# Kernel tuning notes

Hardware: AMD Instinct MI355X
Metric: run time of the kernel (lower is better)

Reference implementation:

```python
import jax, jax.numpy as jnp
import numpy as np

GROUPS = 8   # GroupNorm groups
TOP_K = 2    # top-k routing
TEMP = 1.0   # gate temperature
EPS_GN = 1e-5


def conv1d(x, w, b=None):
    # x: (B,C,T), w: (Cout,Cin,K) -> (B,Cout,T), 'same' padding
    pad = (w.shape[-1] - 1) // 2
    y = jax.lax.conv_general_dilated(x, w, (1,), [(pad, pad)],
                                     dimension_numbers=('NCH', 'OIH', 'NCH'))
    return y if b is None else y + b[None, :, None]


def group_norm(x, gamma, beta, groups=GROUPS, eps=EPS_GN):
    B, C, T = x.shape
    xg = x.reshape(B, groups, C // groups, T)
    mu = xg.mean((2, 3), keepdims=True)
    var = xg.var((2, 3), keepdims=True)
    xn = ((xg - mu) * jax.lax.rsqrt(var + eps)).reshape(B, C, T)
    return xn * gamma[None, :, None] + beta[None, :, None]


def layer_norm(x, gamma, beta, eps=EPS_GN):
    mu = x.mean(-1, keepdims=True)
    var = x.var(-1, keepdims=True)
    return (x - mu) * jax.lax.rsqrt(var + eps) * gamma + beta


def gelu(x):
    return jax.nn.gelu(x, approximate=False)  # torch nn.GELU default (erf)


def setup_inputs() -> dict:
    key = jax.random.key(0)
    ks = jax.random.split(key, 32)
    B, C, T = 32, 16, 2048
    E, CO, K = 8, 128, 5
    HID, CTX, DIN, DEMB = 128, 64, 8, 16
    GIN = CTX + DEMB
    n = lambda i, shape, s=0.05: jax.random.normal(ks[i], shape, dtype=jnp.float32) * s
    return {
        'x': jax.random.normal(ks[0], (B, C, T), dtype=jnp.float32),
        'demo': jax.random.normal(ks[1], (B, DIN), dtype=jnp.float32),
        # router context CNN (Conv1d no bias -> GroupNorm -> GELU)
        'rw': n(2, (HID, C, K)), 'rg': jnp.ones((HID,), jnp.float32), 'rb': jnp.zeros((HID,), jnp.float32),
        # router MLP: Linear -> LayerNorm -> GELU -> Linear
        'm1_w': n(3, (HID, HID)), 'm1_b': jnp.zeros((HID,), jnp.float32),
        'ln_g': jnp.ones((HID,), jnp.float32), 'ln_b': jnp.zeros((HID,), jnp.float32),
        'm2_w': n(4, (CTX, HID)), 'm2_b': jnp.zeros((CTX,), jnp.float32),
        # demographics embedder: Linear -> LayerNorm -> GELU -> Linear
        'd1_w': n(5, (2 * DEMB, DIN)), 'd1_b': jnp.zeros((2 * DEMB,), jnp.float32),
        'dln_g': jnp.ones((2 * DEMB,), jnp.float32), 'dln_b': jnp.zeros((2 * DEMB,), jnp.float32),
        'd2_w': n(6, (DEMB, 2 * DEMB)), 'd2_b': jnp.zeros((DEMB,), jnp.float32),
        # gate linear
        'g_w': n(7, (E, GIN)), 'g_b': jnp.zeros((E,), jnp.float32),
        # specialised expert CNNs (stacked over E): Conv1d -> GroupNorm -> GELU
        'ew': n(8, (E, CO, C, K)), 'eb': jnp.zeros((E, CO), jnp.float32),
        'eg': jnp.ones((E, CO), jnp.float32), 'ebt': jnp.zeros((E, CO), jnp.float32),
        # shared (always-on) expert CNN
        'sw': n(9, (CO, C, K)), 'sb': jnp.zeros((CO,), jnp.float32),
        'sg': jnp.ones((CO,), jnp.float32), 'sbt': jnp.zeros((CO,), jnp.float32),
    }


def reference(x, demo, rw, rg, rb, m1_w, m1_b, ln_g, ln_b, m2_w, m2_b,
              d1_w, d1_b, dln_g, dln_b, d2_w, d2_b, g_w, g_b,
              ew, eb, eg, ebt, sw, sb, sg, sbt):
    # ---- router: context CNN -> GAP -> MLP -> r (B, CTX)
    h = gelu(group_norm(conv1d(x, rw), rg, rb))
    r = h.mean(-1)  # GAP over time
    r = gelu(layer_norm(r @ m1_w.T + m1_b, ln_g, ln_b))
    r = r @ m2_w.T + m2_b
    # ---- demographics embedding, concat onto routing vector
    d = gelu(layer_norm(demo @ d1_w.T + d1_b, dln_g, dln_b))
    d = d @ d2_w.T + d2_b
    r = jnp.concatenate([r, d], axis=-1)  # (B, CTX+DEMB)
    # ---- gate: softmax + top-k mask + renormalise
    logits = (r @ g_w.T + g_b) / TEMP
    weights_soft = jax.nn.softmax(logits, axis=-1)  # (B, E)
    _, topk_idx = jax.lax.top_k(weights_soft, TOP_K)
    Bn = weights_soft.shape[0]
    mask = jnp.zeros_like(weights_soft).at[jnp.arange(Bn)[:, None], topk_idx].set(1.0)
    wh = weights_soft * mask
    weights_hard = wh / (wh.sum(-1, keepdims=True) + 1e-9)
    # ---- experts (dense compute, top-k-masked combine) + shared expert
    expert = lambda w, b, g, be: gelu(group_norm(conv1d(x, w, b), g, be))
    eo = jax.vmap(expert)(ew, eb, eg, ebt)  # (E, B, CO, T)
    shared = gelu(group_norm(conv1d(x, sw, sb), sg, sbt))  # (B, CO, T)
    out = shared + jnp.einsum('be,ebct->bct', weights_hard, eo)
    return out
```

## Files before the change

kernel.cpp:

```cpp
#include <hip/hip_runtime.h>
#include <math.h>

#define B_    32
#define CIN   16
#define T_    2048
#define NG    8
#define CPG   16
#define HID   128
#define KW    5
#define EPS_  1e-5f

#define NROW  2080
#define ROWS  16
#define NQ    4
#define QT    512
#define QROWS 544

#define SH_EWF  1064960
#define SH_RWF  1175552
#define FO_R0   593920
#define FO_GW   598016
#define FO_GI   598080
#define FO_STE  598144

typedef float f32x4 __attribute__((ext_vector_type(4)));
typedef short s16x8 __attribute__((ext_vector_type(8)));

__device__ __forceinline__ float gelu_fast(float y) {
    float p = y * y;
    float u = y * (0.7978845608028654f + 0.03567740813636141f * p);
    float au = fabsf(u);
    float e = __expf(2.0f * au);
    float th = copysignf(1.0f - 2.0f * __builtin_amdgcn_rcpf(e + 1.0f), u);
    return 0.5f * y * (1.0f + th);
}

__device__ __forceinline__ float gelu_sig(float y) {
    float e = __expf(-1.702f * y);
    return y * __builtin_amdgcn_rcpf(1.0f + e);
}

__device__ __forceinline__ float gelu_erf(float y) {
    return 0.5f * y * (1.0f + erff(y * 0.70710678118654752440f));
}

__device__ __forceinline__ short bf16r(float f) {
    unsigned u = __builtin_bit_cast(unsigned, f);
    u = u + 0x7FFFu + ((u >> 16) & 1u);
    return (short)(u >> 16);
}

__global__ __launch_bounds__(256) void prep_kernel(
    const float* __restrict__ x, const float* __restrict__ rw,
    const float* __restrict__ ew, const float* __restrict__ sw,
    short* __restrict__ wsf)
{
    const int bid = blockIdx.x, tid = threadIdx.x;
    if (bid < 64) {
        const int b = bid >> 1, half = bid & 1;
        const float* xb = x + (size_t)b * CIN * T_;
        short* xtb = wsf + (size_t)b * NROW * ROWS;
        const int t0 = (half * 256 + tid) * 4;

        float v[CIN][4];
        #pragma unroll
        for (int ci = 0; ci < CIN; ++ci)
            *(f32x4*)v[ci] = *(const f32x4*)(xb + ci * T_ + t0);

        #pragma unroll
        for (int tt = 0; tt < 4; ++tt) {
            s16x8 lo, hi;
            #pragma unroll
            for (int ci = 0; ci < 8; ++ci) lo[ci] = bf16r(v[ci][tt]);
            #pragma unroll
            for (int ci = 0; ci < 8; ++ci) hi[ci] = bf16r(v[ci + 8][tt]);
            short* rp = xtb + (size_t)(t0 + tt + 2) * ROWS;
            *(s16x8*)rp = lo;
            *(s16x8*)(rp + 8) = hi;
        }
        if (half == 0 && tid < 32) {
            int r = (tid < 2) ? tid : 2048 + tid;
            s16x8 z = {0, 0, 0, 0, 0, 0, 0, 0};
            short* rp = xtb + (size_t)r * ROWS;
            *(s16x8*)rp = z;
            *(s16x8*)(rp + 8) = z;
        }
    } else if (tid < 64) {
        const int id = bid - 64, l = tid;
        const int n = l & 15, grp = l >> 4;
        const int s_ = grp >> 1, cib = (grp & 1) * 8;
        const float* src;
        short* dst;
        if (id < 72) {
            int es = id / 8, g = id - es * 8;
            src = ((es == 0) ? sw : ew + (size_t)(es - 1) * 128 * (CIN * KW))
                  + (size_t)g * CPG * (CIN * KW);
            dst = wsf + SH_EWF + ((size_t)(es * 8 + g) * 3) * 64 * 8;
        } else {
            int g = id - 72;
            src = rw + (size_t)g * CPG * (CIN * KW);
            dst = wsf + SH_RWF + ((size_t)g * 3) * 64 * 8;
        }
        #pragma unroll
        for (int p = 0; p < 3; ++p) {
            int sh = 2 * p + s_;
            s16x8 a;
            if (sh < 5) {
                const float* wp = src + (size_t)n * (CIN * KW) + cib * KW + sh;
                #pragma unroll
                for (int j = 0; j < 8; ++j) a[j] = bf16r(wp[j * KW]);
            } else {
                #pragma unroll
                for (int j = 0; j < 8; ++j) a[j] = 0;
            }
            *(s16x8*)(dst + ((size_t)p * 64 + l) * 8) = a;
        }
    }
}

__device__ __forceinline__ void stage_xt_full(const short* __restrict__ xtb,
                                              short* __restrict__ xs, int tid)
{
    const s16x8* src = (const s16x8*)xtb;
    s16x8* dst = (s16x8*)xs;
    #pragma unroll
    for (int i = 0; i < 8; ++i)
        dst[tid + i * 512] = src[tid + i * 512];
    int i8 = tid + 8 * 512;
    if (i8 < NROW * 2) dst[i8] = src[i8];
}

__device__ __forceinline__ void stage_xt_q(const short* __restrict__ xtq,
                                           short* __restrict__ xs, int tid)
{
    const s16x8* src = (const s16x8*)xtq;
    s16x8* dst = (s16x8*)xs;
    #pragma unroll
    for (int i = 0; i < 4; ++i)
        dst[tid + i * 256] = src[tid + i * 256];
    int i4 = tid + 4 * 256;
    if (i4 < QROWS * 2) dst[i4] = src[i4];
}

__global__ __launch_bounds__(512, 4) void router_conv_kernel(
    const short* __restrict__ xt, const short* __restrict__ wsf,
    const float* __restrict__ rg, const float* __restrict__ rb,
    float* __restrict__ r0)
{
    __shared__ short xs[NROW * ROWS];
    __shared__ float redS[8], redQ[8];
    __shared__ float rsum[8][CPG];

    const int b = blockIdx.x, g = blockIdx.y;
    const int tid = threadIdx.x;
    const int l = tid & 63, wv = tid >> 6;
    const int n = l & 15, grp = l >> 4;
    const int s_ = grp >> 1;

    stage_xt_full(xt + (size_t)b * NROW * ROWS, xs, tid);

    const short* rwb = wsf + SH_RWF + ((size_t)g * 3) * 64 * 8;
    s16x8 afr0 = *(const s16x8*)(rwb + (0 * 64 + l) * 8);
    s16x8 afr1 = *(const s16x8*)(rwb + (1 * 64 + l) * 8);
    s16x8 afr2 = *(const s16x8*)(rwb + (2 * 64 + l) * 8);
    __syncthreads();

    const int cib = (grp & 1) * 8;
    f32x4 cst[16];
    float sA = 0.f, qA = 0.f;
    #pragma unroll
    for (int tile = 0; tile < 16; ++tile) {
        const int t0 = (wv * 16 + tile) * 16;
        s16x8 bf0 = *(const s16x8*)&xs[(t0 + n + 0 + s_) * ROWS + cib];
        s16x8 bf1 = *(const s16x8*)&xs[(t0 + n + 2 + s_) * ROWS + cib];
        s16x8 bf2 = *(const s16x8*)&xs[(t0 + n + 4 + s_) * ROWS + cib];
        f32x4 c = {0.f, 0.f, 0.f, 0.f};
        c = __builtin_amdgcn_mfma_f32_16x16x32_bf16(afr0, bf0, c, 0, 0, 0);
        c = __builtin_amdgcn_mfma_f32_16x16x32_bf16(afr1, bf1, c, 0, 0, 0);
        c = __builtin_amdgcn_mfma_f32_16x16x32_bf16(afr2, bf2, c, 0, 0, 0);
        cst[tile] = c;
        #pragma unroll
        for (int r = 0; r < 4; ++r) { sA += c[r]; qA += c[r] * c[r]; }
    }

    for (int d = 1; d < 64; d <<= 1) {
        sA += __shfl_xor(sA, d);
        qA += __shfl_xor(qA, d);
    }
    if (l == 0) { redS[wv] = sA; redQ[wv] = qA; }
    __syncthreads();
    float S = 0.f, Q = 0.f;
    for (int i = 0; i < 8; ++i) { S += redS[i]; Q += redQ[i]; }
    const float inv_n = 1.0f / (CPG * T_);
    float mu = S * inv_n;
    float rs = rsqrtf(Q * inv_n - mu * mu + EPS_);
    float ka[4], kb[4];
    #pragma unroll
    for (int r = 0; r < 4; ++r) {
        int co = g * CPG + grp * 4 + r;
        float gm = rg[co];
        ka[r] = rs * gm;
        kb[r] = rb[co] - mu * rs * gm;
    }

    f32x4 tacc = {0.f, 0.f, 0.f, 0.f};
    #pragma unroll
    for (int tile = 0; tile < 16; ++tile) {
        #pragma unroll
        for (int r = 0; r < 4; ++r)
            tacc[r] += gelu_fast(cst[tile][r] * ka[r] + kb[r]);
    }
    #pragma unroll
    for (int r = 0; r < 4; ++r)
        for (int d = 1; d < 16; d <<= 1)
            tacc[r] += __shfl_xor(tacc[r], d);
    if (n == 0) {
        #pragma unroll
        for (int r = 0; r < 4; ++r) rsum[wv][grp * 4 + r] = tacc[r];
    }
    __syncthreads();
    if (tid < CPG) {
        float a = 0.f;
        for (int w = 0; w < 8; ++w) a += rsum[w][tid];
        r0[b * HID + g * CPG + tid] = a * (1.0f / T_);
    }
}

__global__ void router_gate_kernel(
    const float* __restrict__ r0, const float* __restrict__ demo,
    const float* __restrict__ m1w, const float* __restrict__ m1b,
    const float* __restrict__ lng, const float* __restrict__ lnb,
    const float* __restrict__ m2w, const float* __restrict__ m2b,
    const float* __restrict__ d1w, const float* __restrict__ d1b,
    const float* __restrict__ dlng, const float* __restrict__ dlnb,
    const float* __restrict__ d2w, const float* __restrict__ d2b,
    const float* __restrict__ gw, const float* __restrict__ gb,
    float* __restrict__ gateW, int* __restrict__ gateI)
{
    __shared__ float sh[128];
    __shared__ float dd[32];
    __shared__ float rr[80];
    __shared__ float glds[8];
    __shared__ float red[2], redq[2];

    const int b = blockIdx.x;
    const int j = threadIdx.x;
    const int lane = j & 63, wv = j >> 6;

    sh[j] = r0[b * HID + j];
    __syncthreads();

    float v = m1b[j];
    for (int i = 0; i < 128; ++i) v += sh[i] * m1w[j * 128 + i];
    float s = v, sq = v * v;
    for (int d = 1; d < 64; d <<= 1) { s += __shfl_xor(s, d); sq += __shfl_xor(sq, d); }
    if (lane == 0) { red[wv] = s; redq[wv] = sq; }
    __syncthreads();
    float S = red[0] + red[1], SQ = redq[0] + redq[1];
    float mu = S * (1.f / 128.f), var = SQ * (1.f / 128.f) - mu * mu;
    float h = (v - mu) * rsqrtf(var + EPS_) * lng[j] + lnb[j];
    float gv = gelu_erf(h);
    __syncthreads();
    sh[j] = gv;
    __syncthreads();

    if (j < 64) {
        float rv = m2b[j];
        for (int i = 0; i < 128; ++i) rv += sh[i] * m2w[j * 128 + i];
        rr[j] = rv;
    } else if (j < 96) {
        int jd = j - 64;
        float u = d1b[jd];
        for (int i = 0; i < 8; ++i) u += demo[b * 8 + i] * d1w[jd * 8 + i];
        float s2 = u, q2 = u * u;
        for (int d = 1; d < 32; d <<= 1) { s2 += __shfl_xor(s2, d, 32); q2 += __shfl_xor(q2, d, 32); }
        float mu2 = s2 * (1.f / 32.f), var2 = q2 * (1.f / 32.f) - mu2 * mu2;
        float y = (u - mu2) * rsqrtf(var2 + EPS_) * dlng[jd] + dlnb[jd];
        dd[jd] = gelu_erf(y);
    }
    __syncthreads();
    if (j < 16) {
        float rv = d2b[j];
        for (int i = 0; i < 32; ++i) rv += dd[i] * d2w[j * 32 + i];
        rr[64 + j] = rv;
    }
    __syncthreads();
    if (j < 8) {
        float lg = gb[j];
        for (int i = 0; i < 80; ++i) lg += rr[i] * gw[j * 80 + i];
        glds[j] = lg;
    }
    __syncthreads();
    if (j == 0) {
        float wsf[8];
        float m = glds[0];
        for (int e = 1; e < 8; ++e) m = fmaxf(m, glds[e]);
        float ssum = 0.f;
        for (int e = 0; e < 8; ++e) { wsf[e] = expf(glds[e] - m); ssum += wsf[e]; }
        for (int e = 0; e < 8; ++e) wsf[e] /= ssum;
        int i1 = 0;
        for (int e = 1; e < 8; ++e) if (wsf[e] > wsf[i1]) i1 = e;
        int i2 = (i1 == 0) ? 1 : 0;
        for (int e = 0; e < 8; ++e) if (e != i1 && wsf[e] > wsf[i2]) i2 = e;
        float a = wsf[i1], b2 = wsf[i2];
        float dn = a + b2 + 1e-9f;
        gateW[b * 2 + 0] = a / dn;
        gateW[b * 2 + 1] = b2 / dn;
        gateI[b * 2 + 0] = i1;
        gateI[b * 2 + 1] = i2;
    }
}

__global__ __launch_bounds__(256, 4) void expert_stats_kernel(
    const short* __restrict__ xt, const short* __restrict__ wsf,
    const float* __restrict__ eb, const float* __restrict__ sb,
    const int* __restrict__ gateI, float* __restrict__ ste)
{
    __shared__ short xs[QROWS * ROWS];

    const int b = blockIdx.x, g = blockIdx.y, q = blockIdx.z;
    const int tid = threadIdx.x;
    const int l = tid & 63, wv = tid >> 6;
    const int n = l & 15, grp = l >> 4;
    const int s_ = grp >> 1, cib = (grp & 1) * 8;

    const int e1 = gateI[b * 2 + 0], e2 = gateI[b * 2 + 1];

    stage_xt_q(xt + ((size_t)b * NROW + q * QT) * ROWS, xs, tid);

    s16x8 afr[3][3];
    const int esi[3] = {0, 1 + e1, 1 + e2};
    #pragma unroll
    for (int sl = 0; sl < 3; ++sl) {
        const short* wb = wsf + SH_EWF + ((size_t)(esi[sl] * 8 + g) * 3) * 64 * 8;
        #pragma unroll
        for (int p = 0; p < 3; ++p)
            afr[sl][p] = *(const s16x8*)(wb + ((size_t)p * 64 + l) * 8);
    }
    float bia[3][4];
    #pragma unroll
    for (int sl = 0; sl < 3; ++sl) {
        const float* bs = (sl == 0) ? sb : eb + ((sl == 1) ? e1 : e2) * 128;
        #pragma unroll
        for (int r = 0; r < 4; ++r) bia[sl][r] = bs[g * CPG + grp * 4 + r];
    }
    __syncthreads();

    float sA[3] = {0.f, 0.f, 0.f}, qA[3] = {0.f, 0.f, 0.f};
    #pragma unroll 2
    for (int tile = 0; tile < 8; ++tile) {
        const int t0 = (wv * 8 + tile) * 16;
        s16x8 bf0 = *(const s16x8*)&xs[(t0 + n + 0 + s_) * ROWS + cib];
        s16x8 bf1 = *(const s16x8*)&xs[(t0 + n + 2 + s_) * ROWS + cib];
        s16x8 bf2 = *(const s16x8*)&xs[(t0 + n + 4 + s_) * ROWS + cib];
        #pragma unroll
        for (int sl = 0; sl < 3; ++sl) {
            f32x4 c = {0.f, 0.f, 0.f, 0.f};
            c = __builtin_amdgcn_mfma_f32_16x16x32_bf16(afr[sl][0], bf0, c, 0, 0, 0);
            c = __builtin_amdgcn_mfma_f32_16x16x32_bf16(afr[sl][1], bf1, c, 0, 0, 0);
            c = __builtin_amdgcn_mfma_f32_16x16x32_bf16(afr[sl][2], bf2, c, 0, 0, 0);
            #pragma unroll
            for (int r = 0; r < 4; ++r) {
                float v = c[r] + bia[sl][r];
                sA[sl] += v; qA[sl] += v * v;
            }
        }
    }
    #pragma unroll
    for (int sl = 0; sl < 3; ++sl)
        for (int d = 1; d < 64; d <<= 1) {
            sA[sl] += __shfl_xor(sA[sl], d);
            qA[sl] += __shfl_xor(qA[sl], d);
        }
    if (l == 0) {
        #pragma unroll
        for (int sl = 0; sl < 3; ++sl) {
            int idx = ((b * NG + g) * 3 + sl) * 16 + q * 4 + wv;
            ste[idx * 2 + 0] = sA[sl];
            ste[idx * 2 + 1] = qA[sl];
        }
    }
}

__global__ __launch_bounds__(256, 4) void expert_apply_kernel(
    const short* __restrict__ xt, const short* __restrict__ wsf,
    const float* __restrict__ eb, const float* __restrict__ eg,
    const float* __restrict__ ebt,
    const float* __restrict__ sb, const float* __restrict__ sg,
    const float* __restrict__ sbt,
    const float* __restrict__ gateW, const int* __restrict__ gateI,
    const float* __restrict__ ste, float* __restrict__ out)
{
    __shared__ short xs[QROWS * ROWS];

    const int b = blockIdx.x, g = blockIdx.y, q = blockIdx.z;
    const int tid = threadIdx.x;
    const int l = tid & 63, wv = tid >> 6;
    const int n = l & 15, grp = l >> 4;
    const int s_ = grp >> 1, cib = (grp & 1) * 8;

    const int e1 = gateI[b * 2 + 0], e2 = gateI[b * 2 + 1];
    const float scl[3] = {1.0f, gateW[b * 2 + 0], gateW[b * 2 + 1]};

    stage_xt_q(xt + ((size_t)b * NROW + q * QT) * ROWS, xs, tid);

    s16x8 afr[3][3];
    const int esi[3] = {0, 1 + e1, 1 + e2};
    #pragma unroll
    for (int sl = 0; sl < 3; ++sl) {
        const short* wb = wsf + SH_EWF + ((size_t)(esi[sl] * 8 + g) * 3) * 64 * 8;
        #pragma unroll
        for (int p = 0; p < 3; ++p)
            afr[sl][p] = *(const s16x8*)(wb + ((size_t)p * 64 + l) * 8);
    }

    const float inv_n = 1.0f / (CPG * T_);
    float ka[3][4], kb[3][4];
    #pragma unroll
    for (int sl = 0; sl < 3; ++sl) {
        float S = 0.f, Q = 0.f;
        const float* sp = ste + (((size_t)(b * NG + g) * 3 + sl) * 16) * 2;
        for (int i = 0; i < 16; ++i) { S += sp[i * 2]; Q += sp[i * 2 + 1]; }
        float mu = S * inv_n;
        float rs = rsqrtf(Q * inv_n - mu * mu + EPS_);
        int e = (sl == 1) ? e1 : e2;
        const float* bs = (sl == 0) ? sb  : eb  + e * 128;
        const float* gs = (sl == 0) ? sg  : eg  + e * 128;
        const float* bt = (sl == 0) ? sbt : ebt + e * 128;
        #pragma unroll
        for (int r = 0; r < 4; ++r) {
            int co = g * CPG + grp * 4 + r;
            float gm = gs[co];
            ka[sl][r] = rs * gm;
            kb[sl][r] = (bs[co] - mu) * rs * gm + bt[co];
        }
    }
    __syncthreads();

    #pragma unroll 2
    for (int tile = 0; tile < 8; ++tile) {
        const int t0 = (wv * 8 + tile) * 16;
        s16x8 bf0 = *(const s16x8*)&xs[(t0 + n + 0 + s_) * ROWS + cib];
        s16x8 bf1 = *(const s16x8*)&xs[(t0 + n + 2 + s_) * ROWS + cib];
        s16x8 bf2 = *(const s16x8*)&xs[(t0 + n + 4 + s_) * ROWS + cib];
        f32x4 oacc = {0.f, 0.f, 0.f, 0.f};
        #pragma unroll
        for (int sl = 0; sl < 3; ++sl) {
            f32x4 c = {0.f, 0.f, 0.f, 0.f};
            c = __builtin_amdgcn_mfma_f32_16x16x32_bf16(afr[sl][0], bf0, c, 0, 0, 0);
            c = __builtin_amdgcn_mfma_f32_16x16x32_bf16(afr[sl][1], bf1, c, 0, 0, 0);
            c = __builtin_amdgcn_mfma_f32_16x16x32_bf16(afr[sl][2], bf2, c, 0, 0, 0);
            #pragma unroll
            for (int r = 0; r < 4; ++r)
                oacc[r] += scl[sl] * gelu_sig(c[r] * ka[sl][r] + kb[sl][r]);
        }
        size_t obase = ((size_t)(b * HID + g * CPG + grp * 4)) * T_
                     + q * QT + t0 + n;
        #pragma unroll
        for (int r = 0; r < 4; ++r)
            out[obase + (size_t)r * T_] = oacc[r];
    }
}

extern "C" void kernel_launch(void* const* d_in, const int* in_sizes, int n_in,
                              void* d_out, int out_size, void* d_ws, size_t ws_size,
                              hipStream_t stream)
{
    const float* x    = (const float*)d_in[0];
    const float* demo = (const float*)d_in[1];
    const float* rw   = (const float*)d_in[2];
    const float* rg   = (const float*)d_in[3];
    const float* rb   = (const float*)d_in[4];
    const float* m1w  = (const float*)d_in[5];
    const float* m1b  = (const float*)d_in[6];
    const float* lng  = (const float*)d_in[7];
    const float* lnb  = (const float*)d_in[8];
    const float* m2w  = (const float*)d_in[9];
    const float* m2b  = (const float*)d_in[10];
    const float* d1w  = (const float*)d_in[11];
    const float* d1b  = (const float*)d_in[12];
    const float* dlng = (const float*)d_in[13];
    const float* dlnb = (const float*)d_in[14];
    const float* d2w  = (const float*)d_in[15];
    const float* d2b  = (const float*)d_in[16];
    const float* gw   = (const float*)d_in[17];
    const float* gb   = (const float*)d_in[18];
    const float* ew   = (const float*)d_in[19];
    const float* eb   = (const float*)d_in[20];
    const float* eg   = (const float*)d_in[21];
    const float* ebt  = (const float*)d_in[22];
    const float* sw   = (const float*)d_in[23];
    const float* sb   = (const float*)d_in[24];
    const float* sg   = (const float*)d_in[25];
    const float* sbt  = (const float*)d_in[26];
    float* out = (float*)d_out;

    short* xt   = (short*)d_ws;
    short* wsfs = (short*)d_ws;
    float* wsff = (float*)d_ws;
    float* r0    = wsff + FO_R0;
    float* gateW = wsff + FO_GW;
    int*   gateI = (int*)wsff + FO_GI;
    float* ste   = wsff + FO_STE;

    prep_kernel<<<dim3(144), 256, 0, stream>>>(x, rw, ew, sw, wsfs);
    dim3 gridc(B_, NG);
    router_conv_kernel<<<gridc, 512, 0, stream>>>(xt, wsfs, rg, rb, r0);
    router_gate_kernel<<<dim3(B_), 128, 0, stream>>>(
        r0, demo, m1w, m1b, lng, lnb, m2w, m2b,
        d1w, d1b, dlng, dlnb, d2w, d2b, gw, gb, gateW, gateI);
    dim3 gridq(B_, NG, NQ);
    expert_stats_kernel<<<gridq, 256, 0, stream>>>(xt, wsfs, eb, sb, gateI, ste);
    expert_apply_kernel<<<gridq, 256, 0, stream>>>(
        xt, wsfs, eb, eg, ebt, sb, sg, sbt, gateW, gateI, ste, out);
    (void)in_sizes; (void)n_in; (void)out_size; (void)ws_size;
}
```

Before: 49.73 us.

## Compute GroupNorm stats for all experts up front, split router conv across quarters

Stats for the router conv, the shared expert and all 8 experts are now computed in one wide kernel (grid B×G×12) before gating, so the stats pass no longer waits on the gate's top-k. The router conv is split into a stats pass plus a per-quarter GAP kernel, which raises parallelism beyond the previous 256 blocks of 512 threads. In exchange the stats kernel does dense conv work for all 8 experts instead of only the 2 selected ones, roughly tripling the stats MFMA work. The router conv is also computed twice, once for stats and once for GAP.

```diff
diff --git a/kernel.cpp b/kernel.cpp
--- a/kernel.cpp
+++ b/kernel.cpp
@@ -16,12 +16,14 @@
 #define QT    512
 #define QROWS 544
 
+#define NSL   10
+
 #define SH_EWF  1064960
 #define SH_RWF  1175552
-#define FO_R0   593920
-#define FO_GW   598016
-#define FO_GI   598080
-#define FO_STE  598144
+#define FO_GW   593920
+#define FO_GI   593984
+#define FO_STE  594048
+#define FO_GAP  675968
 
 typedef float f32x4 __attribute__((ext_vector_type(4)));
 typedef short s16x8 __attribute__((ext_vector_type(8)));
@@ -118,18 +120,6 @@
     }
 }
 
-__device__ __forceinline__ void stage_xt_full(const short* __restrict__ xtb,
-                                              short* __restrict__ xs, int tid)
-{
-    const s16x8* src = (const s16x8*)xtb;
-    s16x8* dst = (s16x8*)xs;
-    #pragma unroll
-    for (int i = 0; i < 8; ++i)
-        dst[tid + i * 512] = src[tid + i * 512];
-    int i8 = tid + 8 * 512;
-    if (i8 < NROW * 2) dst[i8] = src[i8];
-}
-
 __device__ __forceinline__ void stage_xt_q(const short* __restrict__ xtq,
                                            short* __restrict__ xs, int tid)
 {
@@ -142,55 +132,108 @@
     if (i4 < QROWS * 2) dst[i4] = src[i4];
 }
 
-__global__ __launch_bounds__(512, 4) void router_conv_kernel(
+__global__ __launch_bounds__(256, 4) void allstats_kernel(
     const short* __restrict__ xt, const short* __restrict__ wsf,
-    const float* __restrict__ rg, const float* __restrict__ rb,
-    float* __restrict__ r0)
-{
-    __shared__ short xs[NROW * ROWS];
-    __shared__ float redS[8], redQ[8];
-    __shared__ float rsum[8][CPG];
+    const float* __restrict__ eb, const float* __restrict__ sb,
+    float* __restrict__ ste)
+{
+    __shared__ short xs[QROWS * ROWS];
 
     const int b = blockIdx.x, g = blockIdx.y;
+    const int c = blockIdx.z % 3, q = blockIdx.z / 3;
     const int tid = threadIdx.x;
     const int l = tid & 63, wv = tid >> 6;
     const int n = l & 15, grp = l >> 4;
-    const int s_ = grp >> 1;
-
-    stage_xt_full(xt + (size_t)b * NROW * ROWS, xs, tid);
+    const int s_ = grp >> 1, cib = (grp & 1) * 8;
+    const int nsl = (c == 2) ? 2 : 4;
+
+    stage_xt_q(xt + ((size_t)b * NROW + q * QT) * ROWS, xs, tid);
+
+    s16x8 afr[4][3];
+    float bia[4][4];
+    #pragma unroll
+    for (int j = 0; j < 4; ++j) {
+        int usl = c * 4 + j;
+        if (usl > 9) usl = 9;
+        const short* wb = (usl == 0)
+            ? wsf + SH_RWF + ((size_t)g * 3) * 64 * 8
+            : wsf + SH_EWF + ((size_t)((usl - 1) * 8 + g) * 3) * 64 * 8;
+        #pragma unroll
+        for (int p = 0; p < 3; ++p)
+            afr[j][p] = *(const s16x8*)(wb + ((size_t)p * 64 + l) * 8);
+        #pragma unroll
+        for (int r = 0; r < 4; ++r) {
+            if (usl == 0)      bia[j][r] = 0.0f;
+            else if (usl == 1) bia[j][r] = sb[g * CPG + grp * 4 + r];
+            else               bia[j][r] = eb[(usl - 2) * 128 + g * CPG + grp * 4 + r];
+        }
+    }
+    __syncthreads();
+
+    float sA[4] = {0.f, 0.f, 0.f, 0.f}, qA[4] = {0.f, 0.f, 0.f, 0.f};
+    #pragma unroll 2
+    for (int tile = 0; tile < 8; ++tile) {
+        const int t0 = (wv * 8 + tile) * 16;
+        s16x8 bf0 = *(const s16x8*)&xs[(t0 + n + 0 + s_) * ROWS + cib];
+        s16x8 bf1 = *(const s16x8*)&xs[(t0 + n + 2 + s_) * ROWS + cib];
+        s16x8 bf2 = *(const s16x8*)&xs[(t0 + n + 4 + s_) * ROWS + cib];
+        #pragma unroll
+        for (int j = 0; j < 4; ++j) {
+            f32x4 cc = {0.f, 0.f, 0.f, 0.f};
+            cc = __builtin_amdgcn_mfma_f32_16x16x32_bf16(afr[j][0], bf0, cc, 0, 0, 0);
+            cc = __builtin_amdgcn_mfma_f32_16x16x32_bf16(afr[j][1], bf1, cc, 0, 0, 0);
+            cc = __builtin_amdgcn_mfma_f32_16x16x32_bf16(afr[j][2], bf2, cc, 0, 0, 0);
+            #pragma unroll
+            for (int r = 0; r < 4; ++r) {
+                float v = cc[r] + bia[j][r];
+                sA[j] += v; qA[j] += v * v;
+            }
+        }
+    }
+    #pragma unroll
+    for (int j = 0; j < 4; ++j)
+        for (int d = 1; d < 64; d <<= 1) {
+            sA[j] += __shfl_xor(sA[j], d);
+            qA[j] += __shfl_xor(qA[j], d);
+        }
+    if (l == 0) {
+        #pragma unroll
+        for (int j = 0; j < 4; ++j) {
+            if (j < nsl) {
+                int usl = c * 4 + j;
+                int idx = ((b * NG + g) * NSL + usl) * 16 + q * 4 + wv;
+                ste[idx * 2 + 0] = sA[j];
+                ste[idx * 2 + 1] = qA[j];
+            }
+        }
+    }
+}
+
+__global__ __launch_bounds__(256, 4) void router_gap_kernel(
+    const short* __restrict__ xt, const short* __restrict__ wsf,
+    const float* __restrict__ rg, const float* __restrict__ rb,
+    const float* __restrict__ ste, float* __restrict__ gap)
+{
+    __shared__ short xs[QROWS * ROWS];
+
+    const int b = blockIdx.x, g = blockIdx.y, q = blockIdx.z;
+    const int tid = threadIdx.x;
+    const int l = tid & 63, wv = tid >> 6;
+    const int n = l & 15, grp = l >> 4;
+    const int s_ = grp >> 1, cib = (grp & 1) * 8;
+
+    stage_xt_q(xt + ((size_t)b * NROW + q * QT) * ROWS, xs, tid);
 
     const short* rwb = wsf + SH_RWF + ((size_t)g * 3) * 64 * 8;
     s16x8 afr0 = *(const s16x8*)(rwb + (0 * 64 + l) * 8);
     s16x8 afr1 = *(const s16x8*)(rwb + (1 * 64 + l) * 8);
     s16x8 afr2 = *(const s16x8*)(rwb + (2 * 64 + l) * 8);
-    __syncthreads();
-
-    const int cib = (grp & 1) * 8;
-    f32x4 cst[16];
-    float sA = 0.f, qA = 0.f;
-    #pragma unroll
-    for (int tile = 0; tile < 16; ++tile) {
-        const int t0 = (wv * 16 + tile) * 16;
-        s16x8 bf0 = *(const s16x8*)&xs[(t0 + n + 0 + s_) * ROWS + cib];
-        s16x8 bf1 = *(const s16x8*)&xs[(t0 + n + 2 + s_) * ROWS + cib];
-        s16x8 bf2 = *(const s16x8*)&xs[(t0 + n + 4 + s_) * ROWS + cib];
-        f32x4 c = {0.f, 0.f, 0.f, 0.f};
-        c = __builtin_amdgcn_mfma_f32_16x16x32_bf16(afr0, bf0, c, 0, 0, 0);
-        c = __builtin_amdgcn_mfma_f32_16x16x32_bf16(afr1, bf1, c, 0, 0, 0);
-        c = __builtin_amdgcn_mfma_f32_16x16x32_bf16(afr2, bf2, c, 0, 0, 0);
-        cst[tile] = c;
-        #pragma unroll
-        for (int r = 0; r < 4; ++r) { sA += c[r]; qA += c[r] * c[r]; }
-    }
-
-    for (int d = 1; d < 64; d <<= 1) {
-        sA += __shfl_xor(sA, d);
-        qA += __shfl_xor(qA, d);
-    }
-    if (l == 0) { redS[wv] = sA; redQ[wv] = qA; }
-    __syncthreads();
+
     float S = 0.f, Q = 0.f;
-    for (int i = 0; i < 8; ++i) { S += redS[i]; Q += redQ[i]; }
+    {
+        const float* sp = ste + ((size_t)(b * NG + g) * NSL + 0) * 16 * 2;
+        for (int i = 0; i < 16; ++i) { S += sp[i * 2]; Q += sp[i * 2 + 1]; }
+    }
     const float inv_n = 1.0f / (CPG * T_);
     float mu = S * inv_n;
     float rs = rsqrtf(Q * inv_n - mu * mu + EPS_);
@@ -202,13 +245,22 @@
         ka[r] = rs * gm;
         kb[r] = rb[co] - mu * rs * gm;
     }
+    __syncthreads();
 
     f32x4 tacc = {0.f, 0.f, 0.f, 0.f};
-    #pragma unroll
-    for (int tile = 0; tile < 16; ++tile) {
+    #pragma unroll 2
+    for (int tile = 0; tile < 8; ++tile) {
+        const int t0 = (wv * 8 + tile) * 16;
+        s16x8 bf0 = *(const s16x8*)&xs[(t0 + n + 0 + s_) * ROWS + cib];
+        s16x8 bf1 = *(const s16x8*)&xs[(t0 + n + 2 + s_) * ROWS + cib];
+        s16x8 bf2 = *(const s16x8*)&xs[(t0 + n + 4 + s_) * ROWS + cib];
+        f32x4 cc = {0.f, 0.f, 0.f, 0.f};
+        cc = __builtin_amdgcn_mfma_f32_16x16x32_bf16(afr0, bf0, cc, 0, 0, 0);
+        cc = __builtin_amdgcn_mfma_f32_16x16x32_bf16(afr1, bf1, cc, 0, 0, 0);
+        cc = __builtin_amdgcn_mfma_f32_16x16x32_bf16(afr2, bf2, cc, 0, 0, 0);
         #pragma unroll
         for (int r = 0; r < 4; ++r)
-            tacc[r] += gelu_fast(cst[tile][r] * ka[r] + kb[r]);
+            tacc[r] += gelu_fast(cc[r] * ka[r] + kb[r]);
     }
     #pragma unroll
     for (int r = 0; r < 4; ++r)
@@ -216,18 +268,15 @@
             tacc[r] += __shfl_xor(tacc[r], d);
     if (n == 0) {
         #pragma unroll
-        for (int r = 0; r < 4; ++r) rsum[wv][grp * 4 + r] = tacc[r];
-    }
-    __syncthreads();
-    if (tid < CPG) {
-        float a = 0.f;
-        for (int w = 0; w < 8; ++w) a += rsum[w][tid];
-        r0[b * HID + g * CPG + tid] = a * (1.0f / T_);
+        for (int r = 0; r < 4; ++r) {
+            int co = g * CPG + grp * 4 + r;
+            gap[(size_t)(b * HID + co) * 16 + q * 4 + wv] = tacc[r];
+        }
     }
 }
 
 __global__ void router_gate_kernel(
-    const float* __restrict__ r0, const float* __restrict__ demo,
+    const float* __restrict__ gap, const float* __restrict__ demo,
     const float* __restrict__ m1w, const float* __restrict__ m1b,
     const float* __restrict__ lng, const float* __restrict__ lnb,
     const float* __restrict__ m2w, const float* __restrict__ m2b,
@@ -247,7 +296,11 @@
     const int j = threadIdx.x;
     const int lane = j & 63, wv = j >> 6;
 
-    sh[j] = r0[b * HID + j];
+    float a = 0.f;
+    const float* gp = gap + (size_t)(b * HID + j) * 16;
+    #pragma unroll
+    for (int i = 0; i < 16; ++i) a += gp[i];
+    sh[j] = a * (1.0f / T_);
     __syncthreads();
 
     float v = m1b[j];
@@ -302,83 +355,12 @@
         for (int e = 1; e < 8; ++e) if (wsf[e] > wsf[i1]) i1 = e;
         int i2 = (i1 == 0) ? 1 : 0;
         for (int e = 0; e < 8; ++e) if (e != i1 && wsf[e] > wsf[i2]) i2 = e;
-        float a = wsf[i1], b2 = wsf[i2];
-        float dn = a + b2 + 1e-9f;
-        gateW[b * 2 + 0] = a / dn;
+        float aa = wsf[i1], b2 = wsf[i2];
+        float dn = aa + b2 + 1e-9f;
+        gateW[b * 2 + 0] = aa / dn;
         gateW[b * 2 + 1] = b2 / dn;
         gateI[b * 2 + 0] = i1;
         gateI[b * 2 + 1] = i2;
-    }
-}
-
-__global__ __launch_bounds__(256, 4) void expert_stats_kernel(
-    const short* __restrict__ xt, const short* __restrict__ wsf,
-    const float* __restrict__ eb, const float* __restrict__ sb,
-    const int* __restrict__ gateI, float* __restrict__ ste)
-{
-    __shared__ short xs[QROWS * ROWS];
-
-    const int b = blockIdx.x, g = blockIdx.y, q = blockIdx.z;
-    const int tid = threadIdx.x;
-    const int l = tid & 63, wv = tid >> 6;
-    const int n = l & 15, grp = l >> 4;
-    const int s_ = grp >> 1, cib = (grp & 1) * 8;
-
-    const int e1 = gateI[b * 2 + 0], e2 = gateI[b * 2 + 1];
-
-    stage_xt_q(xt + ((size_t)b * NROW + q * QT) * ROWS, xs, tid);
-
-    s16x8 afr[3][3];
-    const int esi[3] = {0, 1 + e1, 1 + e2};
-    #pragma unroll
-    for (int sl = 0; sl < 3; ++sl) {
-        const short* wb = wsf + SH_EWF + ((size_t)(esi[sl] * 8 + g) * 3) * 64 * 8;
-        #pragma unroll
-        for (int p = 0; p < 3; ++p)
-            afr[sl][p] = *(const s16x8*)(wb + ((size_t)p * 64 + l) * 8);
-    }
-    float bia[3][4];
-    #pragma unroll
-    for (int sl = 0; sl < 3; ++sl) {
-        const float* bs = (sl == 0) ? sb : eb + ((sl == 1) ? e1 : e2) * 128;
-        #pragma unroll
-        for (int r = 0; r < 4; ++r) bia[sl][r] = bs[g * CPG + grp * 4 + r];
-    }
-    __syncthreads();
-
-    float sA[3] = {0.f, 0.f, 0.f}, qA[3] = {0.f, 0.f, 0.f};
-    #pragma unroll 2
-    for (int tile = 0; tile < 8; ++tile) {
-        const int t0 = (wv * 8 + tile) * 16;
-        s16x8 bf0 = *(const s16x8*)&xs[(t0 + n + 0 + s_) * ROWS + cib];
-        s16x8 bf1 = *(const s16x8*)&xs[(t0 + n + 2 + s_) * ROWS + cib];
-        s16x8 bf2 = *(const s16x8*)&xs[(t0 + n + 4 + s_) * ROWS + cib];
-        #pragma unroll
-        for (int sl = 0; sl < 3; ++sl) {
-            f32x4 c = {0.f, 0.f, 0.f, 0.f};
-            c = __builtin_amdgcn_mfma_f32_16x16x32_bf16(afr[sl][0], bf0, c, 0, 0, 0);
-            c = __builtin_amdgcn_mfma_f32_16x16x32_bf16(afr[sl][1], bf1, c, 0, 0, 0);
-            c = __builtin_amdgcn_mfma_f32_16x16x32_bf16(afr[sl][2], bf2, c, 0, 0, 0);
-            #pragma unroll
-            for (int r = 0; r < 4; ++r) {
-                float v = c[r] + bia[sl][r];
-                sA[sl] += v; qA[sl] += v * v;
-            }
-        }
-    }
-    #pragma unroll
-    for (int sl = 0; sl < 3; ++sl)
-        for (int d = 1; d < 64; d <<= 1) {
-            sA[sl] += __shfl_xor(sA[sl], d);
-            qA[sl] += __shfl_xor(qA[sl], d);
-        }
-    if (l == 0) {
-        #pragma unroll
-        for (int sl = 0; sl < 3; ++sl) {
-            int idx = ((b * NG + g) * 3 + sl) * 16 + q * 4 + wv;
-            ste[idx * 2 + 0] = sA[sl];
-            ste[idx * 2 + 1] = qA[sl];
-        }
     }
 }
 
@@ -414,12 +396,13 @@
             afr[sl][p] = *(const s16x8*)(wb + ((size_t)p * 64 + l) * 8);
     }
 
+    const int usl[3] = {1, 2 + e1, 2 + e2};
     const float inv_n = 1.0f / (CPG * T_);
     float ka[3][4], kb[3][4];
     #pragma unroll
     for (int sl = 0; sl < 3; ++sl) {
         float S = 0.f, Q = 0.f;
-        const float* sp = ste + (((size_t)(b * NG + g) * 3 + sl) * 16) * 2;
+        const float* sp = ste + ((size_t)(b * NG + g) * NSL + usl[sl]) * 16 * 2;
         for (int i = 0; i < 16; ++i) { S += sp[i * 2]; Q += sp[i * 2 + 1]; }
         float mu = S * inv_n;
         float rs = rsqrtf(Q * inv_n - mu * mu + EPS_);
@@ -446,13 +429,13 @@
         f32x4 oacc = {0.f, 0.f, 0.f, 0.f};
         #pragma unroll
         for (int sl = 0; sl < 3; ++sl) {
-            f32x4 c = {0.f, 0.f, 0.f, 0.f};
-            c = __builtin_amdgcn_mfma_f32_16x16x32_bf16(afr[sl][0], bf0, c, 0, 0, 0);
-            c = __builtin_amdgcn_mfma_f32_16x16x32_bf16(afr[sl][1], bf1, c, 0, 0, 0);
-            c = __builtin_amdgcn_mfma_f32_16x16x32_bf16(afr[sl][2], bf2, c, 0, 0, 0);
+            f32x4 cc = {0.f, 0.f, 0.f, 0.f};
+            cc = __builtin_amdgcn_mfma_f32_16x16x32_bf16(afr[sl][0], bf0, cc, 0, 0, 0);
+            cc = __builtin_amdgcn_mfma_f32_16x16x32_bf16(afr[sl][1], bf1, cc, 0, 0, 0);
+            cc = __builtin_amdgcn_mfma_f32_16x16x32_bf16(afr[sl][2], bf2, cc, 0, 0, 0);
             #pragma unroll
             for (int r = 0; r < 4; ++r)
-                oacc[r] += scl[sl] * gelu_sig(c[r] * ka[sl][r] + kb[sl][r]);
+                oacc[r] += scl[sl] * gelu_sig(cc[r] * ka[sl][r] + kb[sl][r]);
         }
         size_t obase = ((size_t)(b * HID + g * CPG + grp * 4)) * T_
                      + q * QT + t0 + n;
@@ -498,20 +481,18 @@
     short* xt   = (short*)d_ws;
     short* wsfs = (short*)d_ws;
     float* wsff = (float*)d_ws;
-    float* r0    = wsff + FO_R0;
     float* gateW = wsff + FO_GW;
     int*   gateI = (int*)wsff + FO_GI;
     float* ste   = wsff + FO_STE;
+    float* gap   = wsff + FO_GAP;
 
     prep_kernel<<<dim3(144), 256, 0, stream>>>(x, rw, ew, sw, wsfs);
-    dim3 gridc(B_, NG);
-    router_conv_kernel<<<gridc, 512, 0, stream>>>(xt, wsfs, rg, rb, r0);
+    allstats_kernel<<<dim3(B_, NG, NQ * 3), 256, 0, stream>>>(xt, wsfs, eb, sb, ste);
+    router_gap_kernel<<<dim3(B_, NG, NQ), 256, 0, stream>>>(xt, wsfs, rg, rb, ste, gap);
     router_gate_kernel<<<dim3(B_), 128, 0, stream>>>(
-        r0, demo, m1w, m1b, lng, lnb, m2w, m2b,
+        gap, demo, m1w, m1b, lng, lnb, m2w, m2b,
         d1w, d1b, dlng, dlnb, d2w, d2b, gw, gb, gateW, gateI);
-    dim3 gridq(B_, NG, NQ);
-    expert_stats_kernel<<<gridq, 256, 0, stream>>>(xt, wsfs, eb, sb, gateI, ste);
-    expert_apply_kernel<<<gridq, 256, 0, stream>>>(
+    expert_apply_kernel<<<dim3(B_, NG, NQ), 256, 0, stream>>>(
         xt, wsfs, eb, eg, ebt, sb, sg, sbt, gateW, gateI, ste, out);
     (void)in_sizes; (void)n_in; (void)out_size; (void)ws_size;
 }
```

Result: slower. 79.19 us (+59.2%).

## Compute shared-expert GroupNorm stats in router conv kernel; nontemporal output stores

Applied to the files above, without the earlier changes.

The shared expert's GroupNorm sum and sum-of-squares statistics are now computed in the router conv kernel. That kernel already has x staged in LDS, so it runs an extra three MFMAs per tile against the shared-expert weights. The expert_stats kernel then handles only the two routed experts, and expert_apply reads the shared stats from a new workspace slot. Output stores also become nontemporal to avoid polluting the cache. The trade-off is more MFMA work and register pressure in the router kernel, which has only 256 blocks, in exchange for less work in the stats kernel.

```diff
diff --git a/kernel.cpp b/kernel.cpp
--- a/kernel.cpp
+++ b/kernel.cpp
@@ -22,6 +22,7 @@
 #define FO_GW   598016
 #define FO_GI   598080
 #define FO_STE  598144
+#define FO_STSH 614528
 
 typedef float f32x4 __attribute__((ext_vector_type(4)));
 typedef short s16x8 __attribute__((ext_vector_type(8)));
@@ -145,10 +146,11 @@
 __global__ __launch_bounds__(512, 4) void router_conv_kernel(
     const short* __restrict__ xt, const short* __restrict__ wsf,
     const float* __restrict__ rg, const float* __restrict__ rb,
-    float* __restrict__ r0)
+    const float* __restrict__ sb,
+    float* __restrict__ r0, float* __restrict__ stsh)
 {
     __shared__ short xs[NROW * ROWS];
-    __shared__ float redS[8], redQ[8];
+    __shared__ float redS[8], redQ[8], redSS[8], redQS[8];
     __shared__ float rsum[8][CPG];
 
     const int b = blockIdx.x, g = blockIdx.y;
@@ -163,11 +165,18 @@
     s16x8 afr0 = *(const s16x8*)(rwb + (0 * 64 + l) * 8);
     s16x8 afr1 = *(const s16x8*)(rwb + (1 * 64 + l) * 8);
     s16x8 afr2 = *(const s16x8*)(rwb + (2 * 64 + l) * 8);
+    const short* swb = wsf + SH_EWF + ((size_t)(0 * 8 + g) * 3) * 64 * 8;
+    s16x8 asr0 = *(const s16x8*)(swb + (0 * 64 + l) * 8);
+    s16x8 asr1 = *(const s16x8*)(swb + (1 * 64 + l) * 8);
+    s16x8 asr2 = *(const s16x8*)(swb + (2 * 64 + l) * 8);
+    float bsh[4];
+    #pragma unroll
+    for (int r = 0; r < 4; ++r) bsh[r] = sb[g * CPG + grp * 4 + r];
     __syncthreads();
 
     const int cib = (grp & 1) * 8;
     f32x4 cst[16];
-    float sA = 0.f, qA = 0.f;
+    float sA = 0.f, qA = 0.f, sS = 0.f, qS = 0.f;
     #pragma unroll
     for (int tile = 0; tile < 16; ++tile) {
         const int t0 = (wv * 16 + tile) * 16;
@@ -179,18 +188,35 @@
         c = __builtin_amdgcn_mfma_f32_16x16x32_bf16(afr1, bf1, c, 0, 0, 0);
         c = __builtin_amdgcn_mfma_f32_16x16x32_bf16(afr2, bf2, c, 0, 0, 0);
         cst[tile] = c;
-        #pragma unroll
-        for (int r = 0; r < 4; ++r) { sA += c[r]; qA += c[r] * c[r]; }
+        f32x4 cs = {0.f, 0.f, 0.f, 0.f};
+        cs = __builtin_amdgcn_mfma_f32_16x16x32_bf16(asr0, bf0, cs, 0, 0, 0);
+        cs = __builtin_amdgcn_mfma_f32_16x16x32_bf16(asr1, bf1, cs, 0, 0, 0);
+        cs = __builtin_amdgcn_mfma_f32_16x16x32_bf16(asr2, bf2, cs, 0, 0, 0);
+        #pragma unroll
+        for (int r = 0; r < 4; ++r) {
+            sA += c[r]; qA += c[r] * c[r];
+            float v = cs[r] + bsh[r];
+            sS += v; qS += v * v;
+        }
     }
 
     for (int d = 1; d < 64; d <<= 1) {
-        sA += __shfl_xor(sA, d);
-        qA += __shfl_xor(qA, d);
-    }
-    if (l == 0) { redS[wv] = sA; redQ[wv] = qA; }
+        sA += __shfl_xor(sA, d); qA += __shfl_xor(qA, d);
+        sS += __shfl_xor(sS, d); qS += __shfl_xor(qS, d);
+    }
+    if (l == 0) {
+        redS[wv] = sA; redQ[wv] = qA;
+        redSS[wv] = sS; redQS[wv] = qS;
+    }
     __syncthreads();
     float S = 0.f, Q = 0.f;
     for (int i = 0; i < 8; ++i) { S += redS[i]; Q += redQ[i]; }
+    if (tid == 0) {
+        float SS = 0.f, QS = 0.f;
+        for (int i = 0; i < 8; ++i) { SS += redSS[i]; QS += redQS[i]; }
+        stsh[(b * NG + g) * 2 + 0] = SS;
+        stsh[(b * NG + g) * 2 + 1] = QS;
+    }
     const float inv_n = 1.0f / (CPG * T_);
     float mu = S * inv_n;
     float rs = rsqrtf(Q * inv_n - mu * mu + EPS_);
@@ -313,7 +339,7 @@
 
 __global__ __launch_bounds__(256, 4) void expert_stats_kernel(
     const short* __restrict__ xt, const short* __restrict__ wsf,
-    const float* __restrict__ eb, const float* __restrict__ sb,
+    const float* __restrict__ eb,
     const int* __restrict__ gateI, float* __restrict__ ste)
 {
     __shared__ short xs[QROWS * ROWS];
@@ -328,25 +354,25 @@
 
     stage_xt_q(xt + ((size_t)b * NROW + q * QT) * ROWS, xs, tid);
 
-    s16x8 afr[3][3];
-    const int esi[3] = {0, 1 + e1, 1 + e2};
-    #pragma unroll
-    for (int sl = 0; sl < 3; ++sl) {
+    s16x8 afr[2][3];
+    const int esi[2] = {1 + e1, 1 + e2};
+    #pragma unroll
+    for (int sl = 0; sl < 2; ++sl) {
         const short* wb = wsf + SH_EWF + ((size_t)(esi[sl] * 8 + g) * 3) * 64 * 8;
         #pragma unroll
         for (int p = 0; p < 3; ++p)
             afr[sl][p] = *(const s16x8*)(wb + ((size_t)p * 64 + l) * 8);
     }
-    float bia[3][4];
-    #pragma unroll
-    for (int sl = 0; sl < 3; ++sl) {
-        const float* bs = (sl == 0) ? sb : eb + ((sl == 1) ? e1 : e2) * 128;
+    float bia[2][4];
+    #pragma unroll
+    for (int sl = 0; sl < 2; ++sl) {
+        const float* bs = eb + ((sl == 0) ? e1 : e2) * 128;
         #pragma unroll
         for (int r = 0; r < 4; ++r) bia[sl][r] = bs[g * CPG + grp * 4 + r];
     }
     __syncthreads();
 
-    float sA[3] = {0.f, 0.f, 0.f}, qA[3] = {0.f, 0.f, 0.f};
+    float sA[2] = {0.f, 0.f}, qA[2] = {0.f, 0.f};
     #pragma unroll 2
     for (int tile = 0; tile < 8; ++tile) {
         const int t0 = (wv * 8 + tile) * 16;
@@ -354,7 +380,7 @@
         s16x8 bf1 = *(const s16x8*)&xs[(t0 + n + 2 + s_) * ROWS + cib];
         s16x8 bf2 = *(const s16x8*)&xs[(t0 + n + 4 + s_) * ROWS + cib];
         #pragma unroll
-        for (int sl = 0; sl < 3; ++sl) {
+        for (int sl = 0; sl < 2; ++sl) {
             f32x4 c = {0.f, 0.f, 0.f, 0.f};
             c = __builtin_amdgcn_mfma_f32_16x16x32_bf16(afr[sl][0], bf0, c, 0, 0, 0);
             c = __builtin_amdgcn_mfma_f32_16x16x32_bf16(afr[sl][1], bf1, c, 0, 0, 0);
@@ -367,15 +393,15 @@
         }
     }
     #pragma unroll
-    for (int sl = 0; sl < 3; ++sl)
+    for (int sl = 0; sl < 2; ++sl)
         for (int d = 1; d < 64; d <<= 1) {
             sA[sl] += __shfl_xor(sA[sl], d);
             qA[sl] += __shfl_xor(qA[sl], d);
         }
     if (l == 0) {
         #pragma unroll
-        for (int sl = 0; sl < 3; ++sl) {
-            int idx = ((b * NG + g) * 3 + sl) * 16 + q * 4 + wv;
+        for (int sl = 0; sl < 2; ++sl) {
+            int idx = ((b * NG + g) * 2 + sl) * 16 + q * 4 + wv;
             ste[idx * 2 + 0] = sA[sl];
             ste[idx * 2 + 1] = qA[sl];
         }
@@ -389,7 +415,8 @@
     const float* __restrict__ sb, const float* __restrict__ sg,
     const float* __restrict__ sbt,
     const float* __restrict__ gateW, const int* __restrict__ gateI,
-    const float* __restrict__ ste, float* __restrict__ out)
+    const float* __restrict__ ste, const float* __restrict__ stsh,
+    float* __restrict__ out)
 {
     __shared__ short xs[QROWS * ROWS];
 
@@ -418,9 +445,15 @@
     float ka[3][4], kb[3][4];
     #pragma unroll
     for (int sl = 0; sl < 3; ++sl) {
-        float S = 0.f, Q = 0.f;
-        const float* sp = ste + (((size_t)(b * NG + g) * 3 + sl) * 16) * 2;
-        for (int i = 0; i < 16; ++i) { S += sp[i * 2]; Q += sp[i * 2 + 1]; }
+        float S, Q;
+        if (sl == 0) {
+            S = stsh[(b * NG + g) * 2 + 0];
+            Q = stsh[(b * NG + g) * 2 + 1];
+        } else {
+            S = 0.f; Q = 0.f;
+            const float* sp = ste + (((size_t)(b * NG + g) * 2 + (sl - 1)) * 16) * 2;
+            for (int i = 0; i < 16; ++i) { S += sp[i * 2]; Q += sp[i * 2 + 1]; }
+        }
         float mu = S * inv_n;
         float rs = rsqrtf(Q * inv_n - mu * mu + EPS_);
         int e = (sl == 1) ? e1 : e2;
@@ -458,7 +491,7 @@
                      + q * QT + t0 + n;
         #pragma unroll
         for (int r = 0; r < 4; ++r)
-            out[obase + (size_t)r * T_] = oacc[r];
+            __builtin_nontemporal_store(oacc[r], &out[obase + (size_t)r * T_]);
     }
 }
 
@@ -502,16 +535,17 @@
     float* gateW = wsff + FO_GW;
     int*   gateI = (int*)wsff + FO_GI;
     float* ste   = wsff + FO_STE;
+    float* stsh  = wsff + FO_STSH;
 
     prep_kernel<<<dim3(144), 256, 0, stream>>>(x, rw, ew, sw, wsfs);
     dim3 gridc(B_, NG);
-    router_conv_kernel<<<gridc, 512, 0, stream>>>(xt, wsfs, rg, rb, r0);
+    router_conv_kernel<<<gridc, 512, 0, stream>>>(xt, wsfs, rg, rb, sb, r0, stsh);
     router_gate_kernel<<<dim3(B_), 128, 0, stream>>>(
         r0, demo, m1w, m1b, lng, lnb, m2w, m2b,
         d1w, d1b, dlng, dlnb, d2w, d2b, gw, gb, gateW, gateI);
     dim3 gridq(B_, NG, NQ);
-    expert_stats_kernel<<<gridq, 256, 0, stream>>>(xt, wsfs, eb, sb, gateI, ste);
+    expert_stats_kernel<<<gridq, 256, 0, stream>>>(xt, wsfs, eb, gateI, ste);
     expert_apply_kernel<<<gridq, 256, 0, stream>>>(
-        xt, wsfs, eb, eg, ebt, sb, sg, sbt, gateW, gateI, ste, out);
+        xt, wsfs, eb, eg, ebt, sb, sg, sbt, gateW, gateI, ste, stsh, out);
     (void)in_sizes; (void)n_in; (void)out_size; (void)ws_size;
 }
```

Result: faster. 44.43 us (-10.7%).
